# Optimization experiments

Hardware: AMD Instinct MI355X
Metric: run time of the kernel (lower is better)

## Reference

```python
import jax, jax.numpy as jnp
import numpy as np

B, N, K = 8, 2048, 20
EPS = 1e-5  # torch BatchNorm default eps


def knn(x, k):
    # x: (B, C, N). pairwise_distance = -(||xi||^2 - 2 xi.xj + ||xj||^2) (neg sq dist)
    xx = jnp.sum(x * x, axis=1)                      # (B, N)
    inner = jnp.einsum('bcn,bcm->bnm', x, x)         # (B, N, N)
    pd = 2.0 * inner - xx[:, :, None] - xx[:, None, :]
    return jax.lax.top_k(pd, k)[1]                   # (B, N, k) int32 indices


def graph_feature(x, k):
    # x: (B, C, N) -> (B, N, k, 2C) = cat(neighbor - center, center)
    idx = knn(x, k)
    xt = jnp.transpose(x, (0, 2, 1))                 # (B, N, C)
    nbr = jax.vmap(lambda f, i: f[i])(xt, idx)       # (B, N, k, C) per-batch gather
    ctr = xt[:, :, None, :]                          # (B, N, 1, C)
    return jnp.concatenate([nbr - ctr, jnp.broadcast_to(ctr, nbr.shape)], axis=-1)


def edge_conv(x, w, b, g, be, m, v, k):
    # 1x1 Conv2d + BatchNorm (eval: running stats) + ReLU + max over k
    f = graph_feature(x, k)                          # (B, N, k, 2C)
    y = jnp.einsum('bnkc,oc->bonk', f, w) + b[:, None, None]
    y = (y - m[:, None, None]) * (g[:, None, None] / jnp.sqrt(v[:, None, None] + EPS)) + be[:, None, None]
    return jnp.max(jax.nn.relu(y), axis=-1)          # (B, O, N)


def setup_inputs() -> dict:
    key = jax.random.key(0)
    ks = jax.random.split(key, 8)
    x = jax.random.normal(ks[0], (B, 3, N), dtype=jnp.float32)

    def lin(k_, o, i):
        return jax.random.normal(k_, (o, i), dtype=jnp.float32) / np.sqrt(i)

    d = {
        'x': x,
        'w1': lin(ks[1], 64, 6),   'b1': jnp.zeros(64, jnp.float32),
        'g1': jnp.ones(64, jnp.float32), 'be1': jnp.zeros(64, jnp.float32),
        'm1': jnp.zeros(64, jnp.float32), 'v1': jnp.ones(64, jnp.float32),
        'w2': lin(ks[2], 128, 128), 'b2': jnp.zeros(128, jnp.float32),
        'g2': jnp.ones(128, jnp.float32), 'be2': jnp.zeros(128, jnp.float32),
        'm2': jnp.zeros(128, jnp.float32), 'v2': jnp.ones(128, jnp.float32),
        'w3': lin(ks[3], 256, 256), 'b3': jnp.zeros(256, jnp.float32),
        'g3': jnp.ones(256, jnp.float32), 'be3': jnp.zeros(256, jnp.float32),
        'm3': jnp.zeros(256, jnp.float32), 'v3': jnp.ones(256, jnp.float32),
        'wo': lin(ks[4], 512, 448), 'bo': jnp.zeros(512, jnp.float32),
        'go': jnp.ones(512, jnp.float32), 'beo': jnp.zeros(512, jnp.float32),
        'mo': jnp.zeros(512, jnp.float32), 'vo': jnp.ones(512, jnp.float32),
    }
    return d


def reference(x, w1, b1, g1, be1, m1, v1,
              w2, b2, g2, be2, m2, v2,
              w3, b3, g3, be3, m3, v3,
              wo, bo, go, beo, mo, vo):
    x1 = edge_conv(x,  w1, b1, g1, be1, m1, v1, K)   # (B, 64, N)
    x2 = edge_conv(x1, w2, b2, g2, be2, m2, v2, K)   # (B, 128, N)
    x3 = edge_conv(x2, w3, b3, g3, be3, m3, v3, K)   # (B, 256, N)
    h = jnp.concatenate([x1, x2, x3], axis=1)        # (B, 448, N)
    y = jnp.einsum('bcn,oc->bon', h, wo) + bo[:, None]
    y = (y - mo[:, None]) * (go[:, None] / jnp.sqrt(vo[:, None] + EPS)) + beo[:, None]
    y = jax.nn.relu(y)
    return jnp.max(y, axis=2)                        # (B, 512)
```

## Files before the change

### kernel.cpp

```cpp
#include <hip/hip_runtime.h>
#include <hip/hip_bf16.h>
#include <cfloat>

#define BB 8
#define NN 2048
#define KK 20
#define EPSV 1e-5f

typedef __attribute__((ext_vector_type(8))) short bf16x8v;
typedef __attribute__((ext_vector_type(4))) float f32x4v;

__device__ __forceinline__ unsigned short f2bf(float f) {
  unsigned u = __float_as_uint(f);
  return (unsigned short)((u + 0x7fffu + ((u >> 16) & 1u)) >> 16);
}
__device__ __forceinline__ unsigned pack2bf(float a, float b) {
  return (unsigned)f2bf(a) | ((unsigned)f2bf(b) << 16);
}

__global__ __launch_bounds__(256) void pack_x(const float* __restrict__ x,
                                              float* __restrict__ F0,
                                              float* __restrict__ xx) {
  int b = blockIdx.x & 7;
  int n = (blockIdx.x >> 3) * 256 + threadIdx.x;
  if (n >= NN) return;
  float a = x[((size_t)b * 3 + 0) * NN + n];
  float c = x[((size_t)b * 3 + 1) * NN + n];
  float d = x[((size_t)b * 3 + 2) * NN + n];
  size_t r = (size_t)b * NN + n;
  F0[r * 3 + 0] = a;
  F0[r * 3 + 1] = c;
  F0[r * 3 + 2] = d;
  xx[r] = a * a + c * c + d * d;
}

__global__ __launch_bounds__(256) void norms_k(const float* __restrict__ F, int ldf, int C,
                                               float* __restrict__ xx) {
  int b = blockIdx.x & 7;
  int n = (blockIdx.x >> 3) * 256 + threadIdx.x;
  if (n >= NN) return;
  const float* f = F + ((size_t)b * NN + n) * ldf;
  float s = 0.f;
  for (int c = 0; c < C; c += 4) {
    float4 v = *(const float4*)(f + c);
    s += v.x * v.x + v.y * v.y + v.z * v.z + v.w * v.w;
  }
  xx[(size_t)b * NN + n] = s;
}

__global__ __launch_bounds__(256) void transpose_k(const float* __restrict__ src, int lds_, int C,
                                                   float* __restrict__ dst) {
  __shared__ float t[32][33];
  int b = blockIdx.x & 7;
  int tt = blockIdx.x >> 3;
  int n0 = (tt & 63) * 32, c0 = (tt >> 6) * 32;
  int tx = threadIdx.x & 31, ty = threadIdx.x >> 5;
#pragma unroll
  for (int i = 0; i < 32; i += 8) {
    t[ty + i][tx] = src[((size_t)b * NN + n0 + ty + i) * lds_ + c0 + tx];
  }
  __syncthreads();
#pragma unroll
  for (int i = 0; i < 32; i += 8) {
    dst[((size_t)b * C + c0 + ty + i) * NN + n0 + tx] = t[tx][ty + i];
  }
}

__global__ __launch_bounds__(512) void knn1_reg(const float* __restrict__ x,
                                                const float* __restrict__ xx,
                                                int* __restrict__ idx) {
  int b = blockIdx.x & 7;
  int r0 = (blockIdx.x >> 3) * 8;
  int wv = threadIdx.x >> 6, lane = threadIdx.x & 63;
  int r = r0 + wv;
  const float* x0 = x + (size_t)b * 3 * NN;
  const float* x1 = x0 + NN;
  const float* x2 = x0 + 2 * NN;
  const float* xxb = xx + (size_t)b * NN;
  float xr0 = x0[r], xr1 = x1[r], xr2 = x2[r];
  float rn = xxb[r];

  float f[32];
  float v1 = -FLT_MAX, v2 = -FLT_MAX, v3 = -FLT_MAX;
  int m1 = 0x7fffffff, m2 = 0x7fffffff, m3 = 0x7fffffff;
#pragma unroll
  for (int i = 0; i < 32; ++i) {
    int m = i * 64 + lane;
    float acc = xr0 * x0[m];
    acc += xr1 * x1[m];
    acc += xr2 * x2[m];
    float d = (2.f * acc - rn) - xxb[m];
    f[i] = d;
    if (d > v3) {
      if (d > v2) {
        v3 = v2; m3 = m2;
        if (d > v1) { v2 = v1; m2 = m1; v1 = d; m1 = m; }
        else { v2 = d; m2 = m; }
      } else { v3 = d; m3 = m; }
    }
  }

  unsigned used = 0u;
  int navail = 3;
  int myidx = 0;
  for (int it = 0; it < KK; ++it) {
    float bv = v1;
    int bm = m1;
#pragma unroll
    for (int off = 32; off > 0; off >>= 1) {
      float ov = __shfl_xor(bv, off);
      int om = __shfl_xor(bm, off);
      if (ov > bv || (ov == bv && om < bm)) { bv = ov; bm = om; }
    }
    if (lane == it) myidx = bm;
    if (m1 == bm) {
      used |= 1u << (m1 >> 6);
      v1 = v2; m1 = m2;
      v2 = v3; m2 = m3;
      v3 = -FLT_MAX; m3 = 0x7fffffff;
      if (--navail == 0) {
        v1 = v2 = v3 = -FLT_MAX;
        m1 = m2 = m3 = 0x7fffffff;
#pragma unroll
        for (int i = 0; i < 32; ++i) {
          if (used & (1u << i)) continue;
          float v = f[i];
          int m = i * 64 + lane;
          if (v > v3) {
            if (v > v2) {
              v3 = v2; m3 = m2;
              if (v > v1) { v2 = v1; m2 = m1; v1 = v; m1 = m; }
              else { v2 = v; m2 = m; }
            } else { v3 = v; m3 = m; }
          }
        }
        navail = 3;
      }
    }
  }
  if (lane < KK) idx[((size_t)b * NN + r) * KK + lane] = myidx;
}

template <int C>
__global__ __launch_bounds__(256) void dist_gemm(const float* __restrict__ FT,
                                                 const float* __restrict__ xx,
                                                 float* __restrict__ D) {
  __shared__ __align__(16) float Is[8][128];
  __shared__ __align__(16) float Js[8][128];
  int z = blockIdx.z;
  const float* FTb = FT + (size_t)z * C * NN;
  const float* xxb = xx + (size_t)z * NN;
  float* Db = D + (size_t)z * NN * NN;
  int i0 = blockIdx.x * 128, j0 = blockIdx.y * 128;
  int tid = threadIdx.x;
  int tx = tid & 15, ty = tid >> 4;
  int sc = tid >> 5, su = (tid & 31) * 4;

  float acc[8][8];
#pragma unroll
  for (int ii = 0; ii < 8; ++ii)
#pragma unroll
    for (int jj = 0; jj < 8; ++jj) acc[ii][jj] = 0.f;

  for (int c0 = 0; c0 < C; c0 += 8) {
    *(float4*)&Is[sc][su] = *(const float4*)&FTb[(size_t)(c0 + sc) * NN + i0 + su];
    *(float4*)&Js[sc][su] = *(const float4*)&FTb[(size_t)(c0 + sc) * NN + j0 + su];
    __syncthreads();
#pragma unroll
    for (int k = 0; k < 8; ++k) {
      float4 a0 = *(const float4*)&Is[k][tx * 4];
      float4 a1 = *(const float4*)&Is[k][64 + tx * 4];
      float4 b0 = *(const float4*)&Js[k][ty * 4];
      float4 b1 = *(const float4*)&Js[k][64 + ty * 4];
      float ai[8] = {a0.x, a0.y, a0.z, a0.w, a1.x, a1.y, a1.z, a1.w};
      float bj[8] = {b0.x, b0.y, b0.z, b0.w, b1.x, b1.y, b1.z, b1.w};
#pragma unroll
      for (int ii = 0; ii < 8; ++ii)
#pragma unroll
        for (int jj = 0; jj < 8; ++jj) acc[ii][jj] += ai[ii] * bj[jj];
    }
    __syncthreads();
  }

  float4 xi03 = *(const float4*)&xxb[i0 + tx * 4];
  float4 xi47 = *(const float4*)&xxb[i0 + 64 + tx * 4];
  float4 xj03 = *(const float4*)&xxb[j0 + ty * 4];
  float4 xj47 = *(const float4*)&xxb[j0 + 64 + ty * 4];
  float xi[8] = {xi03.x, xi03.y, xi03.z, xi03.w, xi47.x, xi47.y, xi47.z, xi47.w};
  float xj[8] = {xj03.x, xj03.y, xj03.z, xj03.w, xj47.x, xj47.y, xj47.z, xj47.w};
#pragma unroll
  for (int ii = 0; ii < 8; ++ii) {
    int i_ = i0 + (ii < 4 ? tx * 4 + ii : 64 + tx * 4 + (ii - 4));
    float4 o0, o1;
    float* p0 = (float*)&o0;
    float* p1 = (float*)&o1;
#pragma unroll
    for (int jj = 0; jj < 4; ++jj) p0[jj] = (2.f * acc[ii][jj] - xi[ii]) - xj[jj];
#pragma unroll
    for (int jj = 0; jj < 4; ++jj) p1[jj] = (2.f * acc[ii][jj + 4] - xi[ii]) - xj[jj + 4];
    *(float4*)&Db[(size_t)i_ * NN + j0 + ty * 4] = o0;
    *(float4*)&Db[(size_t)i_ * NN + j0 + 64 + ty * 4] = o1;
  }
}

__global__ __launch_bounds__(256) void sel_rows(const float* __restrict__ D,
                                                int* __restrict__ idx) {
  int z = blockIdx.y;
  int wv = threadIdx.x >> 6, lane = threadIdx.x & 63;
  int r = blockIdx.x * 4 + wv;
  const float* row = D + (size_t)z * NN * NN + (size_t)r * NN;

  float f[32];
  float v1 = -FLT_MAX, v2 = -FLT_MAX, v3 = -FLT_MAX;
  int m1 = 0x7fffffff, m2 = 0x7fffffff, m3 = 0x7fffffff;
#pragma unroll
  for (int i = 0; i < 32; ++i) {
    float v = row[i * 64 + lane];
    int m = i * 64 + lane;
    f[i] = v;
    if (v > v3) {
      if (v > v2) {
        v3 = v2; m3 = m2;
        if (v > v1) { v2 = v1; m2 = m1; v1 = v; m1 = m; }
        else { v2 = v; m2 = m; }
      } else { v3 = v; m3 = m; }
    }
  }

  unsigned used = 0u;
  int navail = 3;
  int myidx = 0;
  for (int it = 0; it < KK; ++it) {
    float bv = v1;
    int bm = m1;
#pragma unroll
    for (int off = 32; off > 0; off >>= 1) {
      float ov = __shfl_xor(bv, off);
      int om = __shfl_xor(bm, off);
      if (ov > bv || (ov == bv && om < bm)) { bv = ov; bm = om; }
    }
    if (lane == it) myidx = bm;
    if (m1 == bm) {
      used |= 1u << (m1 >> 6);
      v1 = v2; m1 = m2;
      v2 = v3; m2 = m3;
      v3 = -FLT_MAX; m3 = 0x7fffffff;
      if (--navail == 0) {
        v1 = v2 = v3 = -FLT_MAX;
        m1 = m2 = m3 = 0x7fffffff;
#pragma unroll
        for (int i = 0; i < 32; ++i) {
          if (used & (1u << i)) continue;
          float v = f[i];
          int m = i * 64 + lane;
          if (v > v3) {
            if (v > v2) {
              v3 = v2; m3 = m2;
              if (v > v1) { v2 = v1; m2 = m1; v1 = v; m1 = m; }
              else { v2 = v; m2 = m; }
            } else { v3 = v; m3 = m; }
          }
        }
        navail = 3;
      }
    }
  }
  if (lane < KK) idx[(size_t)z * NN * KK + (size_t)r * KK + lane] = myidx;
}

__global__ __launch_bounds__(256) void prep_edge(const float* __restrict__ w,
                                                 const float* __restrict__ bias,
                                                 const float* __restrict__ g,
                                                 const float* __restrict__ be,
                                                 const float* __restrict__ m,
                                                 const float* __restrict__ v,
                                                 float* __restrict__ Wa, float* __restrict__ Wd,
                                                 float* __restrict__ sv, float* __restrict__ tq,
                                                 int O, int C) {
  int i = blockIdx.x * 256 + threadIdx.x;
  if (i < O * C) {
    int o = i / C, c = i % C;
    float wa = w[(size_t)o * 2 * C + c];
    float wb = w[(size_t)o * 2 * C + C + c];
    Wa[i] = wa;
    Wd[i] = wb - wa;
  }
  if (i < O) {
    float s = g[i] / sqrtf(v[i] + EPSV);
    sv[i] = s;
    tq[i] = (bias[i] - m[i]) * s + be[i];
  }
}

template <bool DUAL>
__global__ __launch_bounds__(256) void gemm_pq(const float* __restrict__ F, int ldf, int C,
                                               const float* __restrict__ Wa,
                                               const float* __restrict__ Wd,
                                               const float* __restrict__ sv,
                                               const float* __restrict__ tp,
                                               const float* __restrict__ tq,
                                               float* __restrict__ P, float* __restrict__ Q,
                                               int O) {
  __shared__ __align__(16) float Fs[8][64];
  __shared__ __align__(16) float Was[8][64];
  __shared__ __align__(16) float Wds[8][64];
  int b = blockIdx.x & 7;
  int tt = blockIdx.x >> 3;
  int n0 = (tt & 31) * 64, o0 = (tt >> 5) * 64;
  int tid = threadIdx.x;
  int tn = tid & 15, to = tid >> 4;
  float accP[4][4] = {{0.f}};
  float accQ[4][4] = {{0.f}};
  const float* Fb = F + (size_t)b * NN * ldf;

  for (int c0 = 0; c0 < C; c0 += 8) {
    for (int e = tid; e < 512; e += 256) {
      int n = e >> 3, k = e & 7, c = c0 + k;
      Fs[k][n] = (c < C) ? Fb[(size_t)(n0 + n) * ldf + c] : 0.f;
      Was[k][n] = (c < C) ? Wa[(size_t)(o0 + n) * C + c] : 0.f;
      if (DUAL) Wds[k][n] = (c < C) ? Wd[(size_t)(o0 + n) * C + c] : 0.f;
    }
    __syncthreads();
#pragma unroll
    for (int k = 0; k < 8; ++k) {
      float4 fq = *(const float4*)&Fs[k][tn * 4];
      float4 aq = *(const float4*)&Was[k][to * 4];
      float fa[4] = {fq.x, fq.y, fq.z, fq.w};
      float aa[4] = {aq.x, aq.y, aq.z, aq.w};
#pragma unroll
      for (int i = 0; i < 4; ++i)
#pragma unroll
        for (int j = 0; j < 4; ++j) accP[i][j] += fa[i] * aa[j];
      if (DUAL) {
        float4 dq = *(const float4*)&Wds[k][to * 4];
        float da[4] = {dq.x, dq.y, dq.z, dq.w};
#pragma unroll
        for (int i = 0; i < 4; ++i)
#pragma unroll
          for (int j = 0; j < 4; ++j) accQ[i][j] += fa[i] * da[j];
      }
    }
    __syncthreads();
  }

#pragma unroll
  for (int j = 0; j < 4; ++j) {
    int o = o0 + to * 4 + j;
    float s = sv[o];
    float tpv = (tp != nullptr) ? tp[o] : 0.f;
    float tqv = DUAL ? tq[o] : 0.f;
#pragma unroll
    for (int i = 0; i < 4; ++i) {
      int n = n0 + tn * 4 + i;
      size_t base = ((size_t)b * NN + n) * O + o;
      P[base] = accP[i][j] * s + tpv;
      if (DUAL) Q[base] = accQ[i][j] * s + tqv;
    }
  }
}

template <int K, bool DUAL>
__global__ __launch_bounds__(256) void gemm_mfma(const float* __restrict__ A, int lda,
                                                 const float* __restrict__ Bw,
                                                 const float* __restrict__ Dw,
                                                 const float* __restrict__ sv,
                                                 const float* __restrict__ tp,
                                                 const float* __restrict__ tq,
                                                 float* __restrict__ P, float* __restrict__ Q,
                                                 int O) {
  __shared__ unsigned short As[128 * 40];
  __shared__ unsigned short Bs[64 * 40];
  __shared__ unsigned short Ds[64 * 40];
  int b = blockIdx.x & 7;
  int tt = blockIdx.x >> 3;
  int nTN = O >> 6;
  int n0 = (tt / nTN) * 128;
  int o0 = (tt % nTN) * 64;
  int tid = threadIdx.x;
  int wv = tid >> 6, lane = tid & 63;
  int wm = wv & 1, wn = wv >> 1;
  const float* Ab = A + (size_t)b * NN * lda;

  f32x4v accP[4][2];
  f32x4v accQ[4][2];
#pragma unroll
  for (int m = 0; m < 4; ++m)
#pragma unroll
    for (int of = 0; of < 2; ++of) {
      accP[m][of] = (f32x4v){0.f, 0.f, 0.f, 0.f};
      if constexpr (DUAL) accQ[m][of] = (f32x4v){0.f, 0.f, 0.f, 0.f};
    }

  for (int ks = 0; ks < K; ks += 32) {
    for (int i = tid; i < 1024; i += 256) {
      int row = i >> 3, k4 = (i & 7) * 4;
      float4 v = *(const float4*)&Ab[(size_t)(n0 + row) * lda + ks + k4];
      uint2 p;
      p.x = pack2bf(v.x, v.y);
      p.y = pack2bf(v.z, v.w);
      *(uint2*)&As[row * 40 + k4] = p;
    }
    for (int i = tid; i < 512; i += 256) {
      int row = i >> 3, k4 = (i & 7) * 4;
      float4 v = *(const float4*)&Bw[(size_t)(o0 + row) * K + ks + k4];
      uint2 p;
      p.x = pack2bf(v.x, v.y);
      p.y = pack2bf(v.z, v.w);
      *(uint2*)&Bs[row * 40 + k4] = p;
      if constexpr (DUAL) {
        float4 d = *(const float4*)&Dw[(size_t)(o0 + row) * K + ks + k4];
        uint2 q;
        q.x = pack2bf(d.x, d.y);
        q.y = pack2bf(d.z, d.w);
        *(uint2*)&Ds[row * 40 + k4] = q;
      }
    }
    __syncthreads();

    int krow = (lane >> 4) * 8;
    bf16x8v af[4], bfr[2], dfr[2];
#pragma unroll
    for (int m = 0; m < 4; ++m)
      af[m] = *(const bf16x8v*)&As[(wm * 64 + m * 16 + (lane & 15)) * 40 + krow];
#pragma unroll
    for (int of = 0; of < 2; ++of) {
      bfr[of] = *(const bf16x8v*)&Bs[(wn * 32 + of * 16 + (lane & 15)) * 40 + krow];
      if constexpr (DUAL)
        dfr[of] = *(const bf16x8v*)&Ds[(wn * 32 + of * 16 + (lane & 15)) * 40 + krow];
    }
#pragma unroll
    for (int m = 0; m < 4; ++m)
#pragma unroll
      for (int of = 0; of < 2; ++of) {
        accP[m][of] = __builtin_amdgcn_mfma_f32_16x16x32_bf16(af[m], bfr[of], accP[m][of], 0, 0, 0);
        if constexpr (DUAL)
          accQ[m][of] = __builtin_amdgcn_mfma_f32_16x16x32_bf16(af[m], dfr[of], accQ[m][of], 0, 0, 0);
      }
    __syncthreads();
  }

#pragma unroll
  for (int of = 0; of < 2; ++of) {
    int o = o0 + wn * 32 + of * 16 + (lane & 15);
    float s = sv[o];
    float bp = (tp != nullptr) ? tp[o] : 0.f;
    float bq = DUAL ? tq[o] : 0.f;
#pragma unroll
    for (int m = 0; m < 4; ++m) {
#pragma unroll
      for (int r = 0; r < 4; ++r) {
        int n = n0 + wm * 64 + m * 16 + (lane >> 4) * 4 + r;
        size_t base = ((size_t)b * NN + n) * O + o;
        P[base] = accP[m][of][r] * s + bp;
        if constexpr (DUAL) Q[base] = accQ[m][of][r] * s + bq;
      }
    }
  }
}

template <int O>
__global__ __launch_bounds__(256) void gather_max2(const float* __restrict__ P,
                                                   const float* __restrict__ Q,
                                                   const int* __restrict__ idx,
                                                   float* __restrict__ H, int c0) {
  constexpr int NPB = 256 / O;
  int b = blockIdx.x & 7;
  int sub = threadIdx.x / O, o = threadIdx.x % O;
  int n = (blockIdx.x >> 3) * NPB + sub;
  const int* id = idx + ((size_t)b * NN + n) * KK;
  float q = Q[((size_t)b * NN + n) * O + o];
  float best = -FLT_MAX;
#pragma unroll 4
  for (int k = 0; k < KK; ++k) {
    int j = id[k];
    float v = P[((size_t)b * NN + j) * O + o] + q;
    best = fmaxf(best, v);
  }
  best = fmaxf(best, 0.f);
  H[((size_t)b * NN + n) * 448 + c0 + o] = best;
}

__global__ __launch_bounds__(256) void reduce_max_part(const float* __restrict__ Z,
                                                       unsigned* __restrict__ out) {
  int b = blockIdx.x & 7;
  int tt = blockIdx.x >> 3;
  int o = (tt & 1) * 256 + threadIdx.x;
  int n0 = (tt >> 1) * 256;
  float m = 0.f;
  for (int n = n0; n < n0 + 256; ++n) {
    float v = Z[((size_t)b * NN + n) * 512 + o];
    m = fmaxf(m, v);
  }
  atomicMax(&out[(size_t)b * 512 + o], __float_as_uint(m));
}

extern "C" void kernel_launch(void* const* d_in, const int* in_sizes, int n_in,
                              void* d_out, int out_size, void* d_ws, size_t ws_size,
                              hipStream_t stream) {
  const float* x = (const float*)d_in[0];
  const float* w1 = (const float*)d_in[1];
  const float* b1 = (const float*)d_in[2];
  const float* g1 = (const float*)d_in[3];
  const float* be1 = (const float*)d_in[4];
  const float* m1 = (const float*)d_in[5];
  const float* v1 = (const float*)d_in[6];
  const float* w2 = (const float*)d_in[7];
  const float* b2 = (const float*)d_in[8];
  const float* g2 = (const float*)d_in[9];
  const float* be2 = (const float*)d_in[10];
  const float* m2 = (const float*)d_in[11];
  const float* v2 = (const float*)d_in[12];
  const float* w3 = (const float*)d_in[13];
  const float* b3 = (const float*)d_in[14];
  const float* g3 = (const float*)d_in[15];
  const float* be3 = (const float*)d_in[16];
  const float* m3 = (const float*)d_in[17];
  const float* v3 = (const float*)d_in[18];
  const float* wo = (const float*)d_in[19];
  const float* bo = (const float*)d_in[20];
  const float* go = (const float*)d_in[21];
  const float* beo = (const float*)d_in[22];
  const float* mo = (const float*)d_in[23];
  const float* vo = (const float*)d_in[24];

  char* ws = (char*)d_ws;
  float* H = (float*)(ws + 0);
  float* F0 = (float*)(ws + 29360128);
  float* xx = (float*)(ws + 29556736);
  int* idx = (int*)(ws + 29622272);
  float* P = (float*)(ws + 30932992);
  float* Q = (float*)(ws + 47710208);
  float* Wa = (float*)(ws + 64487424);
  float* Wd = (float*)(ws + 64618496);
  float* sv = (float*)(ws + 64749568);
  float* tq = (float*)(ws + 64753664);
  float* Z = P;
  float* FT = Q;

  bool bigws = ws_size >= (size_t)198975488;
  float* Dbuf = bigws ? (float*)(ws + 64757760) : P;

  dim3 blk(256);

  pack_x<<<dim3(8 * 8), blk, 0, stream>>>(x, F0, xx);

  prep_edge<<<dim3(1), blk, 0, stream>>>(w1, b1, g1, be1, m1, v1, Wa, Wd, sv, tq, 64, 3);
  knn1_reg<<<dim3(8 * NN / 8), dim3(512), 0, stream>>>(x, xx, idx);
  gemm_pq<true><<<dim3(8 * 32 * 1), blk, 0, stream>>>(F0, 3, 3, Wa, Wd, sv, nullptr, tq, P, Q, 64);
  gather_max2<64><<<dim3(8 * NN / 4), blk, 0, stream>>>(P, Q, idx, H, 0);
  norms_k<<<dim3(8 * 8), blk, 0, stream>>>(H, 448, 64, xx);

  prep_edge<<<dim3(32), blk, 0, stream>>>(w2, b2, g2, be2, m2, v2, Wa, Wd, sv, tq, 128, 64);
  transpose_k<<<dim3(8 * 64 * 2), blk, 0, stream>>>(H, 448, 64, FT);
  if (bigws) {
    dist_gemm<64><<<dim3(16, 16, BB), blk, 0, stream>>>(FT, xx, Dbuf);
    sel_rows<<<dim3(NN / 4, BB), blk, 0, stream>>>(Dbuf, idx);
  } else {
    for (int bb = 0; bb < BB; ++bb) {
      dist_gemm<64><<<dim3(16, 16, 1), blk, 0, stream>>>(FT + (size_t)bb * 64 * NN,
                                                         xx + (size_t)bb * NN, Dbuf);
      sel_rows<<<dim3(NN / 4, 1), blk, 0, stream>>>(Dbuf, idx + (size_t)bb * NN * KK);
    }
  }
  gemm_pq<true><<<dim3(8 * 32 * 2), blk, 0, stream>>>(H, 448, 64, Wa, Wd, sv, nullptr, tq, P, Q, 128);
  gather_max2<128><<<dim3(8 * NN / 2), blk, 0, stream>>>(P, Q, idx, H, 64);
  norms_k<<<dim3(8 * 8), blk, 0, stream>>>(H + 64, 448, 128, xx);

  prep_edge<<<dim3(128), blk, 0, stream>>>(w3, b3, g3, be3, m3, v3, Wa, Wd, sv, tq, 256, 128);
  transpose_k<<<dim3(8 * 64 * 4), blk, 0, stream>>>(H + 64, 448, 128, FT);
  if (bigws) {
    dist_gemm<128><<<dim3(16, 16, BB), blk, 0, stream>>>(FT, xx, Dbuf);
    sel_rows<<<dim3(NN / 4, BB), blk, 0, stream>>>(Dbuf, idx);
  } else {
    for (int bb = 0; bb < BB; ++bb) {
      dist_gemm<128><<<dim3(16, 16, 1), blk, 0, stream>>>(FT + (size_t)bb * 128 * NN,
                                                          xx + (size_t)bb * NN, Dbuf);
      sel_rows<<<dim3(NN / 4, 1), blk, 0, stream>>>(Dbuf, idx + (size_t)bb * NN * KK);
    }
  }
  gemm_mfma<128, true><<<dim3(8 * 16 * 4), blk, 0, stream>>>(H + 64, 448, Wa, Wd, sv, nullptr, tq, P, Q, 256);
  gather_max2<256><<<dim3(8 * NN), blk, 0, stream>>>(P, Q, idx, H, 192);

  prep_edge<<<dim3(2), blk, 0, stream>>>(nullptr, bo, go, beo, mo, vo, nullptr, nullptr, sv, tq, 512, 0);
  gemm_mfma<448, false><<<dim3(8 * 16 * 8), blk, 0, stream>>>(H, 448, wo, nullptr, sv, tq, nullptr, Z, nullptr, 512);

  hipMemsetAsync(d_out, 0, (size_t)out_size * sizeof(float), stream);
  reduce_max_part<<<dim3(8 * 16), blk, 0, stream>>>(Z, (unsigned*)d_out);
}
```

Before: 689.2 us.

## Double-buffer dist_gemm tiles and remap threads for coalesced distance stores

Adds double-buffered shared tiles with register prefetch of the next channel chunk, so global loads overlap the FMA loop and one barrier per iteration is dropped. It also swaps the thread-to-row/column mapping so consecutive threads write consecutive columns of the large distance matrix, giving coalesced stores. The cost is twice the shared memory and some extra live registers for the prefetch.

```diff
diff --git a/kernel.cpp b/kernel.cpp
--- a/kernel.cpp
+++ b/kernel.cpp
@@ -145,15 +145,15 @@
 __global__ __launch_bounds__(256) void dist_gemm(const float* __restrict__ FT,
                                                  const float* __restrict__ xx,
                                                  float* __restrict__ D) {
-  __shared__ __align__(16) float Is[8][128];
-  __shared__ __align__(16) float Js[8][128];
+  __shared__ __align__(16) float Is[2][8][128];
+  __shared__ __align__(16) float Js[2][8][128];
   int z = blockIdx.z;
   const float* FTb = FT + (size_t)z * C * NN;
   const float* xxb = xx + (size_t)z * NN;
   float* Db = D + (size_t)z * NN * NN;
   int i0 = blockIdx.x * 128, j0 = blockIdx.y * 128;
   int tid = threadIdx.x;
-  int tx = tid & 15, ty = tid >> 4;
+  int tj = tid & 15, ti = tid >> 4;
   int sc = tid >> 5, su = (tid & 31) * 4;
 
   float acc[8][8];
@@ -162,16 +162,28 @@
 #pragma unroll
     for (int jj = 0; jj < 8; ++jj) acc[ii][jj] = 0.f;
 
+  {
+    float4 pi = *(const float4*)&FTb[(size_t)sc * NN + i0 + su];
+    float4 pj = *(const float4*)&FTb[(size_t)sc * NN + j0 + su];
+    *(float4*)&Is[0][sc][su] = pi;
+    *(float4*)&Js[0][sc][su] = pj;
+  }
+  __syncthreads();
+
+  int cur = 0;
   for (int c0 = 0; c0 < C; c0 += 8) {
-    *(float4*)&Is[sc][su] = *(const float4*)&FTb[(size_t)(c0 + sc) * NN + i0 + su];
-    *(float4*)&Js[sc][su] = *(const float4*)&FTb[(size_t)(c0 + sc) * NN + j0 + su];
-    __syncthreads();
+    float4 pi, pj;
+    bool more = (c0 + 8 < C);
+    if (more) {
+      pi = *(const float4*)&FTb[(size_t)(c0 + 8 + sc) * NN + i0 + su];
+      pj = *(const float4*)&FTb[(size_t)(c0 + 8 + sc) * NN + j0 + su];
+    }
 #pragma unroll
     for (int k = 0; k < 8; ++k) {
-      float4 a0 = *(const float4*)&Is[k][tx * 4];
-      float4 a1 = *(const float4*)&Is[k][64 + tx * 4];
-      float4 b0 = *(const float4*)&Js[k][ty * 4];
-      float4 b1 = *(const float4*)&Js[k][64 + ty * 4];
+      float4 a0 = *(const float4*)&Is[cur][k][ti * 4];
+      float4 a1 = *(const float4*)&Is[cur][k][64 + ti * 4];
+      float4 b0 = *(const float4*)&Js[cur][k][tj * 4];
+      float4 b1 = *(const float4*)&Js[cur][k][64 + tj * 4];
       float ai[8] = {a0.x, a0.y, a0.z, a0.w, a1.x, a1.y, a1.z, a1.w};
       float bj[8] = {b0.x, b0.y, b0.z, b0.w, b1.x, b1.y, b1.z, b1.w};
 #pragma unroll
@@ -179,18 +191,23 @@
 #pragma unroll
         for (int jj = 0; jj < 8; ++jj) acc[ii][jj] += ai[ii] * bj[jj];
     }
+    if (more) {
+      *(float4*)&Is[cur ^ 1][sc][su] = pi;
+      *(float4*)&Js[cur ^ 1][sc][su] = pj;
+    }
     __syncthreads();
-  }
-
-  float4 xi03 = *(const float4*)&xxb[i0 + tx * 4];
-  float4 xi47 = *(const float4*)&xxb[i0 + 64 + tx * 4];
-  float4 xj03 = *(const float4*)&xxb[j0 + ty * 4];
-  float4 xj47 = *(const float4*)&xxb[j0 + 64 + ty * 4];
+    cur ^= 1;
+  }
+
+  float4 xi03 = *(const float4*)&xxb[i0 + ti * 4];
+  float4 xi47 = *(const float4*)&xxb[i0 + 64 + ti * 4];
+  float4 xj03 = *(const float4*)&xxb[j0 + tj * 4];
+  float4 xj47 = *(const float4*)&xxb[j0 + 64 + tj * 4];
   float xi[8] = {xi03.x, xi03.y, xi03.z, xi03.w, xi47.x, xi47.y, xi47.z, xi47.w};
   float xj[8] = {xj03.x, xj03.y, xj03.z, xj03.w, xj47.x, xj47.y, xj47.z, xj47.w};
 #pragma unroll
   for (int ii = 0; ii < 8; ++ii) {
-    int i_ = i0 + (ii < 4 ? tx * 4 + ii : 64 + tx * 4 + (ii - 4));
+    int i_ = i0 + (ii < 4 ? ti * 4 + ii : 64 + ti * 4 + (ii - 4));
     float4 o0, o1;
     float* p0 = (float*)&o0;
     float* p1 = (float*)&o1;
@@ -198,8 +215,8 @@
     for (int jj = 0; jj < 4; ++jj) p0[jj] = (2.f * acc[ii][jj] - xi[ii]) - xj[jj];
 #pragma unroll
     for (int jj = 0; jj < 4; ++jj) p1[jj] = (2.f * acc[ii][jj + 4] - xi[ii]) - xj[jj + 4];
-    *(float4*)&Db[(size_t)i_ * NN + j0 + ty * 4] = o0;
-    *(float4*)&Db[(size_t)i_ * NN + j0 + 64 + ty * 4] = o1;
+    *(float4*)&Db[(size_t)i_ * NN + j0 + tj * 4] = o0;
+    *(float4*)&Db[(size_t)i_ * NN + j0 + 64 + tj * 4] = o1;
   }
 }
 
```

Measured after the change: 689.5 us. Within noise of the previous version (+0.0%).
